# Kernel optimization log

Measured on AMD Instinct MI355X. Metric: run time of the kernel, lower is better.

## Reference

```python
import jax, jax.numpy as jnp
import numpy as np

N = 50000      # nodes
E = 500000     # edges (before self-loops)
D = 384        # in_channels == hidden3*6 (residual constraint)
H1, C1 = 4, 96   # conv1: heads, out_channels  -> 384
H2, C2 = 4, 96   # conv2 -> 384
H3, C3 = 6, 64   # conv3 -> 384
B = 64           # graphs in batch
SLOPE = 0.2      # GATConv leaky_relu negative_slope (PyG default)
LN_EPS = 1e-5


def _gat_params(key, fin, heads, c, scale=0.05):
    k1, k2, k3 = jax.random.split(key, 3)
    return dict(
        W=jax.random.normal(k1, (fin, heads * c), jnp.float32) * scale,
        a_src=jax.random.normal(k2, (heads, c), jnp.float32) * scale,
        a_dst=jax.random.normal(k3, (heads, c), jnp.float32) * scale,
        b=jnp.zeros((heads * c,), jnp.float32),
    )


def setup_inputs() -> dict:
    key = jax.random.key(0)
    ks = jax.random.split(key, 8)
    x = jax.random.normal(ks[0], (N, D), jnp.float32)
    edge_index = jax.random.randint(ks[1], (2, E), 0, N).astype(jnp.int64)
    batch = jnp.sort(jax.random.randint(ks[2], (N,), 0, B)).astype(jnp.int64)
    p1 = _gat_params(ks[3], D, H1, C1)
    p2 = _gat_params(ks[4], H1 * C1, H2, C2)
    p3 = _gat_params(ks[5], H2 * C2, H3, C3)
    return {
        'x': x, 'edge_index': edge_index, 'batch': batch,
        'W1': p1['W'], 'a1_src': p1['a_src'], 'a1_dst': p1['a_dst'], 'b1': p1['b'],
        'g1': jnp.ones((H1 * C1,), jnp.float32), 'be1': jnp.zeros((H1 * C1,), jnp.float32),
        'W2': p2['W'], 'a2_src': p2['a_src'], 'a2_dst': p2['a_dst'], 'b2': p2['b'],
        'g2': jnp.ones((H2 * C2,), jnp.float32), 'be2': jnp.zeros((H2 * C2,), jnp.float32),
        'W3': p3['W'], 'a3_src': p3['a_src'], 'a3_dst': p3['a_dst'], 'b3': p3['b'],
    }


def _layer_norm(x, g, b):
    mu = jnp.mean(x, axis=-1, keepdims=True)
    var = jnp.mean(jnp.square(x - mu), axis=-1, keepdims=True)
    return (x - mu) * jax.lax.rsqrt(var + LN_EPS) * g + b


def _gat_conv(x, src, dst, W, a_src, a_dst, b, heads, c):
    # h: [N, H, C] projected features (shared W across heads, PyG-style)
    h = (x @ W).reshape(N, heads, c)
    s_src = jnp.einsum('nhc,hc->nh', h, a_src)   # [N, H]
    s_dst = jnp.einsum('nhc,hc->nh', h, a_dst)
    e = jax.nn.leaky_relu(s_src[src] + s_dst[dst], SLOPE)  # [E', H]
    # segment softmax over incoming edges of each dst (self-loops guarantee coverage)
    e_max = jax.ops.segment_max(e, dst, num_segments=N)
    e = jnp.exp(e - e_max[dst])
    denom = jax.ops.segment_sum(e, dst, num_segments=N)
    alpha = e / (denom[dst] + 1e-16)                        # [E', H]
    out = jax.ops.segment_sum(h[src] * alpha[:, :, None], dst, num_segments=N)
    return out.reshape(N, heads * c) + b


def reference(x, edge_index, batch,
              W1, a1_src, a1_dst, b1, g1, be1,
              W2, a2_src, a2_dst, b2, g2, be2,
              W3, a3_src, a3_dst, b3):
    # PyG GATConv adds self-loops by default
    ar = jnp.arange(N, dtype=edge_index.dtype)
    ei = jnp.concatenate([edge_index, jnp.stack([ar, ar])], axis=1)
    src, dst = ei[0], ei[1]

    x1 = _gat_conv(x, src, dst, W1, a1_src, a1_dst, b1, H1, C1)
    x1 = jax.nn.relu(_layer_norm(x1, g1, be1))
    x2 = _gat_conv(x1, src, dst, W2, a2_src, a2_dst, b2, H2, C2)
    x2 = jax.nn.relu(_layer_norm(x2, g2, be2))
    x3 = _gat_conv(x2, src, dst, W3, a3_src, a3_dst, b3, H3, C3)
    x3 = jax.nn.relu(x3)

    x_res = x + x3
    # global_mean_pool over batch assignment (dropout is identity at eval)
    sums = jax.ops.segment_sum(x_res, batch, num_segments=B)
    counts = jax.ops.segment_sum(jnp.ones((N,), x.dtype), batch, num_segments=B)
    return sums / jnp.maximum(counts, 1.0)[:, None]
```

## Files before the change

### kernel.cpp

```cpp
#include <hip/hip_runtime.h>

#define NNODES 50000
#define NEDGES 500000
#define DIM    384
#define NB     64
#define SLOPE  0.2f
#define LN_EPS 1e-5f
#define EPRIME (NEDGES + NNODES)
#define POOLS  16
#define SCANB  256
#define NSCB   ((NNODES + SCANB - 1) / SCANB)

typedef __attribute__((ext_vector_type(8))) short short8;
typedef __attribute__((ext_vector_type(4))) float floatx4;
typedef __attribute__((ext_vector_type(2))) float floatx2;

__device__ __forceinline__ int load_i(const void* p, long long i, int is64) {
  return is64 ? (int)((const long long*)p)[i] : ((const int*)p)[i];
}
__device__ __forceinline__ unsigned short f2bf(float f) {
  unsigned u = __float_as_uint(f);
  u += 0x7fffu + ((u >> 16) & 1u);
  return (unsigned short)(u >> 16);
}
__device__ __forceinline__ float bf2f(unsigned short u) {
  return __uint_as_float(((unsigned)u) << 16);
}

__global__ void detect_kernel(const int* __restrict__ ei32, int* __restrict__ flag) {
  __shared__ int nz;
  if (threadIdx.x == 0) nz = 0;
  __syncthreads();
  if (ei32[2 * threadIdx.x + 1] != 0) atomicAdd(&nz, 1);
  __syncthreads();
  if (threadIdx.x == 0) *flag = (nz == 0) ? 1 : 0;
}

__global__ void count_kernel(const void* __restrict__ ei, const int* __restrict__ flag,
                             int* __restrict__ deg) {
  int is64 = *flag;
  for (int i = blockIdx.x * blockDim.x + threadIdx.x; i < EPRIME; i += gridDim.x * blockDim.x) {
    int d = (i < NEDGES) ? load_i(ei, (long long)NEDGES + i, is64) : (i - NEDGES);
    atomicAdd(&deg[d], 1);
  }
}

__global__ void scan1_kernel(const int* __restrict__ deg, int* __restrict__ row_ptr,
                             int* __restrict__ btot) {
  __shared__ int buf[SCANB];
  int t = threadIdx.x, idx = blockIdx.x * SCANB + t;
  int v = (idx < NNODES) ? deg[idx] : 0;
  buf[t] = v;
  __syncthreads();
  for (int off = 1; off < SCANB; off <<= 1) {
    int x = (t >= off) ? buf[t - off] : 0;
    __syncthreads();
    buf[t] += x;
    __syncthreads();
  }
  if (idx < NNODES) row_ptr[idx] = buf[t] - v;
  if (t == SCANB - 1) btot[blockIdx.x] = buf[t];
}
__global__ void scan2_kernel(int* __restrict__ btot) {
  __shared__ int buf[256];
  int t = threadIdx.x;
  int v = (t < NSCB) ? btot[t] : 0;
  buf[t] = v;
  __syncthreads();
  for (int off = 1; off < 256; off <<= 1) {
    int x = (t >= off) ? buf[t - off] : 0;
    __syncthreads();
    buf[t] += x;
    __syncthreads();
  }
  if (t < NSCB) btot[t] = buf[t] - v;
}
__global__ void scan3_kernel(int* __restrict__ row_ptr, int* __restrict__ cursor,
                             const int* __restrict__ btot) {
  int idx = blockIdx.x * SCANB + threadIdx.x;
  if (idx < NNODES) {
    int v = row_ptr[idx] + btot[blockIdx.x];
    row_ptr[idx] = v;
    cursor[idx] = v;
  }
  if (idx == 0) row_ptr[NNODES] = EPRIME;
}

__global__ void scatter_kernel(const void* __restrict__ ei, const int* __restrict__ flag,
                               int* __restrict__ cursor, int* __restrict__ srt) {
  int is64 = *flag;
  for (int i = blockIdx.x * blockDim.x + threadIdx.x; i < EPRIME; i += gridDim.x * blockDim.x) {
    int s, d;
    if (i < NEDGES) { s = load_i(ei, i, is64); d = load_i(ei, (long long)NEDGES + i, is64); }
    else            { s = d = i - NEDGES; }
    int pos = atomicAdd(&cursor[d], 1);
    srt[pos] = s;
  }
}

__global__ void convert_x_kernel(const float* __restrict__ x, unsigned short* __restrict__ xb) {
  int i = blockIdx.x * blockDim.x + threadIdx.x;
  float4 v = ((const float4*)x)[i];
  ushort4 o;
  o.x = f2bf(v.x); o.y = f2bf(v.y); o.z = f2bf(v.z); o.w = f2bf(v.w);
  ((ushort4*)xb)[i] = o;
}

__global__ void convert_w_kernel(const float* __restrict__ W1, const float* __restrict__ W2,
                                 const float* __restrict__ W3, unsigned short* __restrict__ Wt) {
  const float* W = (blockIdx.y == 0) ? W1 : (blockIdx.y == 1) ? W2 : W3;
  unsigned short* o = Wt + (size_t)blockIdx.y * DIM * DIM;
  int n = blockIdx.x;
  int k = threadIdx.x;
  o[n * DIM + k] = f2bf(W[k * DIM + n]);
}

__global__ __launch_bounds__(256)
void gemm_bf16_kernel(const unsigned short* __restrict__ A,
                      const unsigned short* __restrict__ Bt,
                      unsigned short* __restrict__ Cb, int M) {
  __shared__ unsigned short As[128 * 32];
  __shared__ unsigned short Bs[128 * 32];
  int tid = threadIdx.x;
  int lane = tid & 63;
  int wave = tid >> 6;
  int bm = blockIdx.x * 128;
  int bn = blockIdx.y * 128;
  int wm = (wave & 1) * 64;
  int wn = (wave >> 1) * 64;
  int l16 = lane & 15;
  int lq  = lane >> 4;

  floatx4 acc[4][4];
#pragma unroll
  for (int mi = 0; mi < 4; ++mi)
#pragma unroll
    for (int ni = 0; ni < 4; ++ni)
      acc[mi][ni] = (floatx4){0.f, 0.f, 0.f, 0.f};

  for (int k0 = 0; k0 < DIM; k0 += 32) {
    __syncthreads();
#pragma unroll
    for (int i = 0; i < 2; ++i) {
      int c = i * 256 + tid;
      int r = c >> 2;
      int col = (c & 3) << 3;
      int ra = bm + r; if (ra >= M) ra = M - 1;
      __builtin_amdgcn_global_load_lds(
          (const __attribute__((address_space(1))) void*)(A + (size_t)ra * DIM + k0 + col),
          (__attribute__((address_space(3))) void*)(As + c * 8), 16, 0, 0);
      __builtin_amdgcn_global_load_lds(
          (const __attribute__((address_space(1))) void*)(Bt + (size_t)(bn + r) * DIM + k0 + col),
          (__attribute__((address_space(3))) void*)(Bs + c * 8), 16, 0, 0);
    }
    __syncthreads();
    short8 av[4], bv[4];
#pragma unroll
    for (int mi = 0; mi < 4; ++mi)
      av[mi] = *(const short8*)&As[(wm + mi * 16 + l16) * 32 + lq * 8];
#pragma unroll
    for (int ni = 0; ni < 4; ++ni)
      bv[ni] = *(const short8*)&Bs[(wn + ni * 16 + l16) * 32 + lq * 8];
#pragma unroll
    for (int mi = 0; mi < 4; ++mi)
#pragma unroll
      for (int ni = 0; ni < 4; ++ni)
        acc[mi][ni] = __builtin_amdgcn_mfma_f32_16x16x32_bf16(av[mi], bv[ni], acc[mi][ni], 0, 0, 0);
  }

#pragma unroll
  for (int mi = 0; mi < 4; ++mi) {
#pragma unroll
    for (int r = 0; r < 4; ++r) {
      int row = bm + wm + mi * 16 + lq * 4 + r;
      if (row < M) {
#pragma unroll
        for (int ni = 0; ni < 4; ++ni)
          Cb[(size_t)row * DIM + bn + wn + ni * 16 + l16] = f2bf(acc[mi][ni][r]);
      }
    }
  }
}

template <int H>
__global__ __launch_bounds__(256)
void score_kernel(const unsigned short* __restrict__ hmat,
                  const float* __restrict__ asrc, const float* __restrict__ adst,
                  float* __restrict__ ssrc, float* __restrict__ sdst,
                  unsigned char* __restrict__ h8) {
  constexpr int LPH = 48 / H;
  int wave = threadIdx.x >> 6, lane = threadIdx.x & 63;
  int n = blockIdx.x * 4 + wave;
  bool colane = lane < 48;
  int lc = min(lane, 47);
  int j = lc * 8;

  __shared__ float r1[4][64], r2[4][64];
  float s1 = 0.f, s2 = 0.f;
  if (colane) {
    uint4 pk = *(const uint4*)(hmat + (size_t)n * DIM + j);
    float f[8];
    f[0] = __uint_as_float(pk.x << 16); f[1] = __uint_as_float(pk.x & 0xffff0000u);
    f[2] = __uint_as_float(pk.y << 16); f[3] = __uint_as_float(pk.y & 0xffff0000u);
    f[4] = __uint_as_float(pk.z << 16); f[5] = __uint_as_float(pk.z & 0xffff0000u);
    f[6] = __uint_as_float(pk.w << 16); f[7] = __uint_as_float(pk.w & 0xffff0000u);
    float4 a0 = *(const float4*)(asrc + j);
    float4 a1 = *(const float4*)(asrc + j + 4);
    float4 d0 = *(const float4*)(adst + j);
    float4 d1 = *(const float4*)(adst + j + 4);
    s1 = f[0]*a0.x + f[1]*a0.y + f[2]*a0.z + f[3]*a0.w
       + f[4]*a1.x + f[5]*a1.y + f[6]*a1.z + f[7]*a1.w;
    s2 = f[0]*d0.x + f[1]*d0.y + f[2]*d0.z + f[3]*d0.w
       + f[4]*d1.x + f[5]*d1.y + f[6]*d1.z + f[7]*d1.w;
    int w0 = __builtin_amdgcn_cvt_pk_fp8_f32(f[0], f[1], 0, false);
    w0 = __builtin_amdgcn_cvt_pk_fp8_f32(f[2], f[3], w0, true);
    int w1 = __builtin_amdgcn_cvt_pk_fp8_f32(f[4], f[5], 0, false);
    w1 = __builtin_amdgcn_cvt_pk_fp8_f32(f[6], f[7], w1, true);
    uint2 st; st.x = (unsigned)w0; st.y = (unsigned)w1;
    *(uint2*)(h8 + (size_t)n * DIM + j) = st;
  }
  r1[wave][lane] = colane ? s1 : 0.f;
  r2[wave][lane] = colane ? s2 : 0.f;
  asm volatile("s_waitcnt lgkmcnt(0)" ::: "memory");
  __builtin_amdgcn_wave_barrier();
  if (lane < H) {
    float a = 0.f;
#pragma unroll
    for (int k = 0; k < LPH; ++k) a += r1[wave][lane * LPH + k];
    ssrc[n * H + lane] = a;
  } else if (lane >= 8 && lane < 8 + H) {
    int h = lane - 8;
    float a = 0.f;
#pragma unroll
    for (int k = 0; k < LPH; ++k) a += r2[wave][h * LPH + k];
    sdst[n * H + h] = a;
  }
}

template <int H, int MODE>
__global__ __launch_bounds__(256)
void aggregate_kernel(const int* __restrict__ row_ptr, const int* __restrict__ srt,
                      const float* __restrict__ ssrc, const float* __restrict__ sdst,
                      const unsigned char* __restrict__ h8, const float* __restrict__ bias,
                      const float* __restrict__ gamma, const float* __restrict__ beta,
                      const float* __restrict__ xres, float* __restrict__ outf,
                      unsigned short* __restrict__ outb) {
  constexpr int C = DIM / H;
  int wave = threadIdx.x >> 6;
  int lane = threadIdx.x & 63;
  int n = blockIdx.x * 4 + wave;
  int start = row_ptr[n];
  int deg = row_ptr[n + 1] - start;

  __shared__ float wexp_all[4][H][68];
  float (*wexp)[68] = wexp_all[wave];

  bool colane = lane < 48;
  int lc = min(lane, 47);
  int j = lc * 8;
  int myhead = j / C;

  float sdn[H];
#pragma unroll
  for (int h = 0; h < H; ++h) sdn[h] = sdst[n * H + h];

  float M[H], S[H];
#pragma unroll
  for (int h = 0; h < H; ++h) { M[h] = -1e30f; S[h] = 0.f; }
  float acc[8];
#pragma unroll
  for (int i = 0; i < 8; ++i) acc[i] = 0.f;

  for (int base = 0; base < deg; base += 64) {
    int cnt = min(64, deg - base);
    int s = 0;
    float sc[H];
    if (lane < cnt) {
      s = srt[start + base + lane];
      if (H == 4) {
        float4 sv = *(const float4*)(ssrc + s * 4);
        float svv[4] = {sv.x, sv.y, sv.z, sv.w};
#pragma unroll
        for (int h = 0; h < 4; ++h) {
          float v = svv[h] + sdn[h];
          sc[h] = fmaxf(v, SLOPE * v);
        }
      } else {
#pragma unroll
        for (int h = 0; h < H; ++h) {
          float v = ssrc[s * H + h] + sdn[h];
          sc[h] = fmaxf(v, SLOPE * v);
        }
      }
    } else {
#pragma unroll
      for (int h = 0; h < H; ++h) sc[h] = -1e30f;
    }
    float cm[H];
#pragma unroll
    for (int h = 0; h < H; ++h) cm[h] = sc[h];
#pragma unroll
    for (int off = 32; off > 0; off >>= 1)
#pragma unroll
      for (int h = 0; h < H; ++h) cm[h] = fmaxf(cm[h], __shfl_xor(cm[h], off));
    float r[H], ex[H];
#pragma unroll
    for (int h = 0; h < H; ++h) {
      float Mn = fmaxf(M[h], cm[h]);
      r[h] = __expf(M[h] - Mn);
      M[h] = Mn;
      ex[h] = __expf(sc[h] - Mn);
      wexp[h][lane] = ex[h];
    }
    asm volatile("s_waitcnt lgkmcnt(0)" ::: "memory");
    __builtin_amdgcn_wave_barrier();
#pragma unroll
    for (int h = 0; h < H; ++h) {
      float cs = ex[h];
#pragma unroll
      for (int off = 32; off > 0; off >>= 1) cs += __shfl_xor(cs, off);
      S[h] = S[h] * r[h] + cs;
    }
    {
      float rr = r[myhead];
#pragma unroll
      for (int i = 0; i < 8; ++i) acc[i] *= rr;
    }

    auto accum = [&](uint2 pk, float w) {
      floatx2 p0 = __builtin_amdgcn_cvt_pk_f32_fp8((int)pk.x, false);
      floatx2 p1 = __builtin_amdgcn_cvt_pk_f32_fp8((int)pk.x, true);
      floatx2 p2 = __builtin_amdgcn_cvt_pk_f32_fp8((int)pk.y, false);
      floatx2 p3 = __builtin_amdgcn_cvt_pk_f32_fp8((int)pk.y, true);
      acc[0] = fmaf(w, p0.x, acc[0]); acc[1] = fmaf(w, p0.y, acc[1]);
      acc[2] = fmaf(w, p1.x, acc[2]); acc[3] = fmaf(w, p1.y, acc[3]);
      acc[4] = fmaf(w, p2.x, acc[4]); acc[5] = fmaf(w, p2.y, acc[5]);
      acc[6] = fmaf(w, p3.x, acc[6]); acc[7] = fmaf(w, p3.y, acc[7]);
    };
    int ee = 0;
    for (; ee + 4 <= cnt; ee += 4) {
      int s0 = __builtin_amdgcn_readfirstlane(__shfl(s, ee));
      int s1 = __builtin_amdgcn_readfirstlane(__shfl(s, ee + 1));
      int s2 = __builtin_amdgcn_readfirstlane(__shfl(s, ee + 2));
      int s3 = __builtin_amdgcn_readfirstlane(__shfl(s, ee + 3));
      uint2 k0 = *(const uint2*)(h8 + (size_t)s0 * DIM + j);
      uint2 k1 = *(const uint2*)(h8 + (size_t)s1 * DIM + j);
      uint2 k2 = *(const uint2*)(h8 + (size_t)s2 * DIM + j);
      uint2 k3 = *(const uint2*)(h8 + (size_t)s3 * DIM + j);
      float w0 = wexp[myhead][ee];
      float w1 = wexp[myhead][ee + 1];
      float w2 = wexp[myhead][ee + 2];
      float w3 = wexp[myhead][ee + 3];
      accum(k0, w0); accum(k1, w1); accum(k2, w2); accum(k3, w3);
    }
    for (; ee < cnt; ++ee) {
      int su = __builtin_amdgcn_readfirstlane(__shfl(s, ee));
      uint2 pk = *(const uint2*)(h8 + (size_t)su * DIM + j);
      accum(pk, wexp[myhead][ee]);
    }
    __builtin_amdgcn_wave_barrier();
  }

  float inv = 1.f / (S[myhead] + 1e-16f);
  float v[8];
  float4 b0 = *(const float4*)(bias + j);
  float4 b1 = *(const float4*)(bias + j + 4);
  v[0] = acc[0] * inv + b0.x; v[1] = acc[1] * inv + b0.y;
  v[2] = acc[2] * inv + b0.z; v[3] = acc[3] * inv + b0.w;
  v[4] = acc[4] * inv + b1.x; v[5] = acc[5] * inv + b1.y;
  v[6] = acc[6] * inv + b1.z; v[7] = acc[7] * inv + b1.w;

  if (MODE == 0) {
    float s1 = 0.f, s2 = 0.f;
    if (colane) {
#pragma unroll
      for (int i = 0; i < 8; ++i) { s1 += v[i]; s2 += v[i] * v[i]; }
    }
#pragma unroll
    for (int off = 32; off > 0; off >>= 1) {
      s1 += __shfl_xor(s1, off);
      s2 += __shfl_xor(s2, off);
    }
    float mu = s1 * (1.f / DIM);
    float var = s2 * (1.f / DIM) - mu * mu;
    float rs = rsqrtf(var + LN_EPS);
    if (colane) {
      float4 g0 = *(const float4*)(gamma + j);
      float4 g1 = *(const float4*)(gamma + j + 4);
      float4 e0 = *(const float4*)(beta + j);
      float4 e1 = *(const float4*)(beta + j + 4);
      float gg[8] = {g0.x, g0.y, g0.z, g0.w, g1.x, g1.y, g1.z, g1.w};
      float bb[8] = {e0.x, e0.y, e0.z, e0.w, e1.x, e1.y, e1.z, e1.w};
      ushort4 o0, o1;
      unsigned short oy[8];
#pragma unroll
      for (int i = 0; i < 8; ++i) {
        float y = (v[i] - mu) * rs * gg[i] + bb[i];
        oy[i] = f2bf(fmaxf(y, 0.f));
      }
      o0.x = oy[0]; o0.y = oy[1]; o0.z = oy[2]; o0.w = oy[3];
      o1.x = oy[4]; o1.y = oy[5]; o1.z = oy[6]; o1.w = oy[7];
      *(ushort4*)(outb + (size_t)n * DIM + j) = o0;
      *(ushort4*)(outb + (size_t)n * DIM + j + 4) = o1;
    }
  } else {
    if (colane) {
      const float* xr = xres + (size_t)n * DIM + j;
      float4 x0 = *(const float4*)xr;
      float4 x1 = *(const float4*)(xr + 4);
      float4 o0, o1;
      o0.x = fmaxf(v[0], 0.f) + x0.x; o0.y = fmaxf(v[1], 0.f) + x0.y;
      o0.z = fmaxf(v[2], 0.f) + x0.z; o0.w = fmaxf(v[3], 0.f) + x0.w;
      o1.x = fmaxf(v[4], 0.f) + x1.x; o1.y = fmaxf(v[5], 0.f) + x1.y;
      o1.z = fmaxf(v[6], 0.f) + x1.z; o1.w = fmaxf(v[7], 0.f) + x1.w;
      float* op = outf + (size_t)n * DIM + j;
      *(float4*)op = o0;
      *(float4*)(op + 4) = o1;
    }
  }
}

__global__ void pool_kernel(const float* __restrict__ xr, const void* __restrict__ batch,
                            const int* __restrict__ flag, float* __restrict__ out) {
  int b = blockIdx.x;
  int s = blockIdx.y;
  int t = threadIdx.x;
  int is64 = *flag;
  int lo, hi;
  { int l = 0, r = NNODES;
    while (l < r) { int m = (l + r) >> 1; if (load_i(batch, m, is64) < b) l = m + 1; else r = m; }
    lo = l; }
  { int l = lo, r = NNODES;
    while (l < r) { int m = (l + r) >> 1; if (load_i(batch, m, is64) < b + 1) l = m + 1; else r = m; }
    hi = l; }
  int cnt = hi - lo;
  float inv = 1.f / (float)max(cnt, 1);
  int chunk = (cnt + POOLS - 1) / POOLS;
  int r0 = lo + s * chunk;
  int r1 = min(r0 + chunk, hi);
  float acc = 0.f;
  for (int nn = r0; nn < r1; ++nn) acc += xr[(size_t)nn * DIM + t];
  if (r1 > r0) atomicAdd(&out[b * DIM + t], acc * inv);
}

extern "C" void kernel_launch(void* const* d_in, const int* in_sizes, int n_in,
                              void* d_out, int out_size, void* d_ws, size_t ws_size,
                              hipStream_t stream) {
  const float* x    = (const float*)d_in[0];
  const void*  ei   = d_in[1];
  const void*  batch= d_in[2];
  const float* W1   = (const float*)d_in[3];
  const float* a1s  = (const float*)d_in[4];
  const float* a1d  = (const float*)d_in[5];
  const float* b1   = (const float*)d_in[6];
  const float* g1   = (const float*)d_in[7];
  const float* be1  = (const float*)d_in[8];
  const float* W2   = (const float*)d_in[9];
  const float* a2s  = (const float*)d_in[10];
  const float* a2d  = (const float*)d_in[11];
  const float* b2   = (const float*)d_in[12];
  const float* g2   = (const float*)d_in[13];
  const float* be2  = (const float*)d_in[14];
  const float* W3   = (const float*)d_in[15];
  const float* a3s  = (const float*)d_in[16];
  const float* a3d  = (const float*)d_in[17];
  const float* b3   = (const float*)d_in[18];
  float* out = (float*)d_out;

  char* ws = (char*)d_ws;
  size_t off = 0;
  auto alloc = [&](size_t bytes) -> void* {
    void* p = ws + off;
    off = (off + bytes + 255) & ~(size_t)255;
    return p;
  };
  int*   flag    = (int*)alloc(4);
  char*  R       = (char*)alloc((size_t)NNODES * DIM * 4);
  unsigned short* Xb = (unsigned short*)R;
  unsigned short* Qb = (unsigned short*)(R + (size_t)NNODES * DIM * 2);
  float* Qf      = (float*)R;
  unsigned short* P = (unsigned short*)alloc((size_t)NNODES * DIM * 2);
  unsigned char*  P8 = (unsigned char*)alloc((size_t)NNODES * DIM);
  unsigned short* Wt = (unsigned short*)alloc((size_t)3 * DIM * DIM * 2);
  float* ssrc    = (float*)alloc((size_t)NNODES * 6 * 4);
  float* sdst    = (float*)alloc((size_t)NNODES * 6 * 4);
  int*   row_ptr = (int*)alloc((size_t)(NNODES + 1) * 4);
  int*   cursor  = (int*)alloc((size_t)NNODES * 4);
  int*   deg     = (int*)alloc((size_t)NNODES * 4);
  int*   btot    = (int*)alloc((size_t)NSCB * 4);
  int*   srt     = (int*)alloc((size_t)EPRIME * 4);

  detect_kernel<<<1, 256, 0, stream>>>((const int*)ei, flag);
  hipMemsetAsync(deg, 0, (size_t)NNODES * 4, stream);
  hipMemsetAsync(d_out, 0, (size_t)out_size * 4, stream);
  int eblocks = (EPRIME + 255) / 256;
  count_kernel<<<eblocks, 256, 0, stream>>>(ei, flag, deg);
  scan1_kernel<<<NSCB, SCANB, 0, stream>>>(deg, row_ptr, btot);
  scan2_kernel<<<1, 256, 0, stream>>>(btot);
  scan3_kernel<<<NSCB, SCANB, 0, stream>>>(row_ptr, cursor, btot);
  scatter_kernel<<<eblocks, 256, 0, stream>>>(ei, flag, cursor, srt);

  convert_x_kernel<<<(NNODES * DIM / 4 + 255) / 256, 256, 0, stream>>>(x, Xb);
  convert_w_kernel<<<dim3(DIM, 3), DIM, 0, stream>>>(W1, W2, W3, Wt);

  dim3 ggrid((NNODES + 127) / 128, DIM / 128);
  int agrid = NNODES / 4;

  gemm_bf16_kernel<<<ggrid, 256, 0, stream>>>(Xb, Wt, P, NNODES);
  score_kernel<4><<<agrid, 256, 0, stream>>>(P, a1s, a1d, ssrc, sdst, P8);
  aggregate_kernel<4, 0><<<agrid, 256, 0, stream>>>(row_ptr, srt, ssrc, sdst, P8, b1, g1, be1,
                                                    nullptr, nullptr, Qb);
  gemm_bf16_kernel<<<ggrid, 256, 0, stream>>>(Qb, Wt + (size_t)DIM * DIM, P, NNODES);
  score_kernel<4><<<agrid, 256, 0, stream>>>(P, a2s, a2d, ssrc, sdst, P8);
  aggregate_kernel<4, 0><<<agrid, 256, 0, stream>>>(row_ptr, srt, ssrc, sdst, P8, b2, g2, be2,
                                                    nullptr, nullptr, Qb);
  gemm_bf16_kernel<<<ggrid, 256, 0, stream>>>(Qb, Wt + (size_t)2 * DIM * DIM, P, NNODES);
  score_kernel<6><<<agrid, 256, 0, stream>>>(P, a3s, a3d, ssrc, sdst, P8);
  aggregate_kernel<6, 1><<<agrid, 256, 0, stream>>>(row_ptr, srt, ssrc, sdst, P8, b3, nullptr,
                                                    nullptr, x, Qf, nullptr);
  pool_kernel<<<dim3(NB, POOLS), DIM, 0, stream>>>(Qf, batch, flag, out);
}
```

Measured before the change: 595.7 us.

## Split edge softmax into separate per-node-head kernel feeding aggregation

The online softmax inside the aggregation kernel is replaced by a separate kernel. It has one thread per (node, head), makes three passes over the node's incoming edges, and writes normalized alpha per edge to global memory. The aggregate kernel then just reads the alpha values and the source indices directly and accumulates, with no shuffles, LDS or rescaling. This removes the wave-level reduction overhead from the gather loop, but adds a kernel launch per layer, an extra global alpha buffer, and three irregular passes over ssrc per (node, head) with poor coalescing.

Result: faster. 578.5 us (-2.9%).

```diff
diff --git a/kernel.cpp b/kernel.cpp
--- a/kernel.cpp
+++ b/kernel.cpp
@@ -22,9 +22,6 @@
   unsigned u = __float_as_uint(f);
   u += 0x7fffu + ((u >> 16) & 1u);
   return (unsigned short)(u >> 16);
-}
-__device__ __forceinline__ float bf2f(unsigned short u) {
-  return __uint_as_float(((unsigned)u) << 16);
 }
 
 __global__ void detect_kernel(const int* __restrict__ ei32, int* __restrict__ flag) {
@@ -237,10 +234,40 @@
   }
 }
 
+template <int H>
+__global__ __launch_bounds__(256)
+void softmax_kernel(const int* __restrict__ row_ptr, const int* __restrict__ srt,
+                    const float* __restrict__ ssrc, const float* __restrict__ sdst,
+                    float* __restrict__ alpha) {
+  int idx = blockIdx.x * 256 + threadIdx.x;
+  if (idx >= NNODES * H) return;
+  int n = idx / H, h = idx - n * H;
+  int start = row_ptr[n], end = row_ptr[n + 1];
+  float sd = sdst[n * H + h];
+  float m = -1e30f;
+  for (int e = start; e < end; ++e) {
+    float v = ssrc[srt[e] * H + h] + sd;
+    v = fmaxf(v, SLOPE * v);
+    m = fmaxf(m, v);
+  }
+  float den = 0.f;
+  for (int e = start; e < end; ++e) {
+    float v = ssrc[srt[e] * H + h] + sd;
+    v = fmaxf(v, SLOPE * v);
+    den += __expf(v - m);
+  }
+  float inv = 1.f / (den + 1e-16f);
+  for (int e = start; e < end; ++e) {
+    float v = ssrc[srt[e] * H + h] + sd;
+    v = fmaxf(v, SLOPE * v);
+    alpha[(size_t)e * H + h] = __expf(v - m) * inv;
+  }
+}
+
 template <int H, int MODE>
 __global__ __launch_bounds__(256)
 void aggregate_kernel(const int* __restrict__ row_ptr, const int* __restrict__ srt,
-                      const float* __restrict__ ssrc, const float* __restrict__ sdst,
+                      const float* __restrict__ alpha,
                       const unsigned char* __restrict__ h8, const float* __restrict__ bias,
                       const float* __restrict__ gamma, const float* __restrict__ beta,
                       const float* __restrict__ xres, float* __restrict__ outf,
@@ -252,123 +279,59 @@
   int start = row_ptr[n];
   int deg = row_ptr[n + 1] - start;
 
-  __shared__ float wexp_all[4][H][68];
-  float (*wexp)[68] = wexp_all[wave];
-
   bool colane = lane < 48;
   int lc = min(lane, 47);
   int j = lc * 8;
   int myhead = j / C;
 
-  float sdn[H];
-#pragma unroll
-  for (int h = 0; h < H; ++h) sdn[h] = sdst[n * H + h];
-
-  float M[H], S[H];
-#pragma unroll
-  for (int h = 0; h < H; ++h) { M[h] = -1e30f; S[h] = 0.f; }
   float acc[8];
 #pragma unroll
   for (int i = 0; i < 8; ++i) acc[i] = 0.f;
 
-  for (int base = 0; base < deg; base += 64) {
-    int cnt = min(64, deg - base);
-    int s = 0;
-    float sc[H];
-    if (lane < cnt) {
-      s = srt[start + base + lane];
-      if (H == 4) {
-        float4 sv = *(const float4*)(ssrc + s * 4);
-        float svv[4] = {sv.x, sv.y, sv.z, sv.w};
-#pragma unroll
-        for (int h = 0; h < 4; ++h) {
-          float v = svv[h] + sdn[h];
-          sc[h] = fmaxf(v, SLOPE * v);
-        }
-      } else {
-#pragma unroll
-        for (int h = 0; h < H; ++h) {
-          float v = ssrc[s * H + h] + sdn[h];
-          sc[h] = fmaxf(v, SLOPE * v);
-        }
-      }
-    } else {
-#pragma unroll
-      for (int h = 0; h < H; ++h) sc[h] = -1e30f;
-    }
-    float cm[H];
-#pragma unroll
-    for (int h = 0; h < H; ++h) cm[h] = sc[h];
-#pragma unroll
-    for (int off = 32; off > 0; off >>= 1)
-#pragma unroll
-      for (int h = 0; h < H; ++h) cm[h] = fmaxf(cm[h], __shfl_xor(cm[h], off));
-    float r[H], ex[H];
-#pragma unroll
-    for (int h = 0; h < H; ++h) {
-      float Mn = fmaxf(M[h], cm[h]);
-      r[h] = __expf(M[h] - Mn);
-      M[h] = Mn;
-      ex[h] = __expf(sc[h] - Mn);
-      wexp[h][lane] = ex[h];
-    }
-    asm volatile("s_waitcnt lgkmcnt(0)" ::: "memory");
-    __builtin_amdgcn_wave_barrier();
-#pragma unroll
-    for (int h = 0; h < H; ++h) {
-      float cs = ex[h];
-#pragma unroll
-      for (int off = 32; off > 0; off >>= 1) cs += __shfl_xor(cs, off);
-      S[h] = S[h] * r[h] + cs;
-    }
-    {
-      float rr = r[myhead];
-#pragma unroll
-      for (int i = 0; i < 8; ++i) acc[i] *= rr;
-    }
-
-    auto accum = [&](uint2 pk, float w) {
-      floatx2 p0 = __builtin_amdgcn_cvt_pk_f32_fp8((int)pk.x, false);
-      floatx2 p1 = __builtin_amdgcn_cvt_pk_f32_fp8((int)pk.x, true);
-      floatx2 p2 = __builtin_amdgcn_cvt_pk_f32_fp8((int)pk.y, false);
-      floatx2 p3 = __builtin_amdgcn_cvt_pk_f32_fp8((int)pk.y, true);
-      acc[0] = fmaf(w, p0.x, acc[0]); acc[1] = fmaf(w, p0.y, acc[1]);
-      acc[2] = fmaf(w, p1.x, acc[2]); acc[3] = fmaf(w, p1.y, acc[3]);
-      acc[4] = fmaf(w, p2.x, acc[4]); acc[5] = fmaf(w, p2.y, acc[5]);
-      acc[6] = fmaf(w, p3.x, acc[6]); acc[7] = fmaf(w, p3.y, acc[7]);
-    };
-    int ee = 0;
-    for (; ee + 4 <= cnt; ee += 4) {
-      int s0 = __builtin_amdgcn_readfirstlane(__shfl(s, ee));
-      int s1 = __builtin_amdgcn_readfirstlane(__shfl(s, ee + 1));
-      int s2 = __builtin_amdgcn_readfirstlane(__shfl(s, ee + 2));
-      int s3 = __builtin_amdgcn_readfirstlane(__shfl(s, ee + 3));
-      uint2 k0 = *(const uint2*)(h8 + (size_t)s0 * DIM + j);
-      uint2 k1 = *(const uint2*)(h8 + (size_t)s1 * DIM + j);
-      uint2 k2 = *(const uint2*)(h8 + (size_t)s2 * DIM + j);
-      uint2 k3 = *(const uint2*)(h8 + (size_t)s3 * DIM + j);
-      float w0 = wexp[myhead][ee];
-      float w1 = wexp[myhead][ee + 1];
-      float w2 = wexp[myhead][ee + 2];
-      float w3 = wexp[myhead][ee + 3];
-      accum(k0, w0); accum(k1, w1); accum(k2, w2); accum(k3, w3);
-    }
-    for (; ee < cnt; ++ee) {
-      int su = __builtin_amdgcn_readfirstlane(__shfl(s, ee));
-      uint2 pk = *(const uint2*)(h8 + (size_t)su * DIM + j);
-      accum(pk, wexp[myhead][ee]);
-    }
-    __builtin_amdgcn_wave_barrier();
-  }
-
-  float inv = 1.f / (S[myhead] + 1e-16f);
+  const int* sp = srt + start;
+  const float* ap = alpha + (size_t)start * H + myhead;
+
+  auto accum = [&](uint2 pk, float w) {
+    floatx2 p0 = __builtin_amdgcn_cvt_pk_f32_fp8((int)pk.x, false);
+    floatx2 p1 = __builtin_amdgcn_cvt_pk_f32_fp8((int)pk.x, true);
+    floatx2 p2 = __builtin_amdgcn_cvt_pk_f32_fp8((int)pk.y, false);
+    floatx2 p3 = __builtin_amdgcn_cvt_pk_f32_fp8((int)pk.y, true);
+    acc[0] = fmaf(w, p0.x, acc[0]); acc[1] = fmaf(w, p0.y, acc[1]);
+    acc[2] = fmaf(w, p1.x, acc[2]); acc[3] = fmaf(w, p1.y, acc[3]);
+    acc[4] = fmaf(w, p2.x, acc[4]); acc[5] = fmaf(w, p2.y, acc[5]);
+    acc[6] = fmaf(w, p3.x, acc[6]); acc[7] = fmaf(w, p3.y, acc[7]);
+  };
+
+  int ee = 0;
+  for (; ee + 4 <= deg; ee += 4) {
+    int i0 = sp[ee], i1 = sp[ee + 1], i2 = sp[ee + 2], i3 = sp[ee + 3];
+    int s0 = __builtin_amdgcn_readfirstlane(i0);
+    int s1 = __builtin_amdgcn_readfirstlane(i1);
+    int s2 = __builtin_amdgcn_readfirstlane(i2);
+    int s3 = __builtin_amdgcn_readfirstlane(i3);
+    uint2 k0 = *(const uint2*)(h8 + (size_t)s0 * DIM + j);
+    uint2 k1 = *(const uint2*)(h8 + (size_t)s1 * DIM + j);
+    uint2 k2 = *(const uint2*)(h8 + (size_t)s2 * DIM + j);
+    uint2 k3 = *(const uint2*)(h8 + (size_t)s3 * DIM + j);
+    float w0 = ap[(ee) * H];
+    float w1 = ap[(ee + 1) * H];
+    float w2 = ap[(ee + 2) * H];
+    float w3 = ap[(ee + 3) * H];
+    accum(k0, w0); accum(k1, w1); accum(k2, w2); accum(k3, w3);
+  }
+  for (; ee < deg; ++ee) {
+    int su = __builtin_amdgcn_readfirstlane(sp[ee]);
+    uint2 pk = *(const uint2*)(h8 + (size_t)su * DIM + j);
+    accum(pk, ap[ee * H]);
+  }
+
   float v[8];
   float4 b0 = *(const float4*)(bias + j);
   float4 b1 = *(const float4*)(bias + j + 4);
-  v[0] = acc[0] * inv + b0.x; v[1] = acc[1] * inv + b0.y;
-  v[2] = acc[2] * inv + b0.z; v[3] = acc[3] * inv + b0.w;
-  v[4] = acc[4] * inv + b1.x; v[5] = acc[5] * inv + b1.y;
-  v[6] = acc[6] * inv + b1.z; v[7] = acc[7] * inv + b1.w;
+  v[0] = acc[0] + b0.x; v[1] = acc[1] + b0.y;
+  v[2] = acc[2] + b0.z; v[3] = acc[3] + b0.w;
+  v[4] = acc[4] + b1.x; v[5] = acc[5] + b1.y;
+  v[6] = acc[6] + b1.z; v[7] = acc[7] + b1.w;
 
   if (MODE == 0) {
     float s1 = 0.f, s2 = 0.f;
@@ -484,6 +447,7 @@
   unsigned short* Wt = (unsigned short*)alloc((size_t)3 * DIM * DIM * 2);
   float* ssrc    = (float*)alloc((size_t)NNODES * 6 * 4);
   float* sdst    = (float*)alloc((size_t)NNODES * 6 * 4);
+  float* alpha   = (float*)alloc((size_t)EPRIME * 6 * 4);
   int*   row_ptr = (int*)alloc((size_t)(NNODES + 1) * 4);
   int*   cursor  = (int*)alloc((size_t)NNODES * 4);
   int*   deg     = (int*)alloc((size_t)NNODES * 4);
@@ -505,18 +469,23 @@
 
   dim3 ggrid((NNODES + 127) / 128, DIM / 128);
   int agrid = NNODES / 4;
+  int smb4 = (NNODES * 4 + 255) / 256;
+  int smb6 = (NNODES * 6 + 255) / 256;
 
   gemm_bf16_kernel<<<ggrid, 256, 0, stream>>>(Xb, Wt, P, NNODES);
   score_kernel<4><<<agrid, 256, 0, stream>>>(P, a1s, a1d, ssrc, sdst, P8);
-  aggregate_kernel<4, 0><<<agrid, 256, 0, stream>>>(row_ptr, srt, ssrc, sdst, P8, b1, g1, be1,
+  softmax_kernel<4><<<smb4, 256, 0, stream>>>(row_ptr, srt, ssrc, sdst, alpha);
+  aggregate_kernel<4, 0><<<agrid, 256, 0, stream>>>(row_ptr, srt, alpha, P8, b1, g1, be1,
                                                     nullptr, nullptr, Qb);
   gemm_bf16_kernel<<<ggrid, 256, 0, stream>>>(Qb, Wt + (size_t)DIM * DIM, P, NNODES);
   score_kernel<4><<<agrid, 256, 0, stream>>>(P, a2s, a2d, ssrc, sdst, P8);
-  aggregate_kernel<4, 0><<<agrid, 256, 0, stream>>>(row_ptr, srt, ssrc, sdst, P8, b2, g2, be2,
+  softmax_kernel<4><<<smb4, 256, 0, stream>>>(row_ptr, srt, ssrc, sdst, alpha);
+  aggregate_kernel<4, 0><<<agrid, 256, 0, stream>>>(row_ptr, srt, alpha, P8, b2, g2, be2,
                                                     nullptr, nullptr, Qb);
   gemm_bf16_kernel<<<ggrid, 256, 0, stream>>>(Qb, Wt + (size_t)2 * DIM * DIM, P, NNODES);
   score_kernel<6><<<agrid, 256, 0, stream>>>(P, a3s, a3d, ssrc, sdst, P8);
-  aggregate_kernel<6, 1><<<agrid, 256, 0, stream>>>(row_ptr, srt, ssrc, sdst, P8, b3, nullptr,
+  softmax_kernel<6><<<smb6, 256, 0, stream>>>(row_ptr, srt, ssrc, sdst, alpha);
+  aggregate_kernel<6, 1><<<agrid, 256, 0, stream>>>(row_ptr, srt, alpha, P8, b3, nullptr,
                                                     nullptr, x, Qf, nullptr);
   pool_kernel<<<dim3(NB, POOLS), DIM, 0, stream>>>(Qf, batch, flag, out);
 }
```
